# Performance work log

Hardware: AMD Instinct MI355X
Metric: run time of the kernel (lower is better)

## Reference

```python
import jax, jax.numpy as jnp
import numpy as np
import math

N_HEAD = 12


def setup_inputs() -> dict:
    key = jax.random.key(0)
    k1, k2, k3 = jax.random.split(key, 3)
    B, T, C = 4, 2048, 768
    x = jax.random.normal(k1, (B, T, C), dtype=jnp.float32)
    W = jax.random.normal(k2, (C, 3 * C), dtype=jnp.float32) * 0.02
    b = jax.random.normal(k3, (3 * C,), dtype=jnp.float32) * 0.02
    return {"x": x, "W": W, "b": b}


def reference(x, W, b):
    B, T, C = x.shape
    H = N_HEAD
    d = C // H
    qkv = x @ W + b                                # [B,T,3C]
    q, k, v = jnp.split(qkv, 3, axis=-1)           # each [B,T,C]
    q = q.reshape(B, T, H, d).transpose(0, 2, 1, 3)  # [B,H,T,d]
    k = k.reshape(B, T, H, d).transpose(0, 2, 1, 3)
    v = v.reshape(B, T, H, d).transpose(0, 2, 1, 3)
    # NOTE: source multiplies by sqrt(d) (not divides) -- faithful reproduction.
    att = jnp.einsum('bhqd,bhkd->bhqk', q, k) * (1.0 * math.sqrt(d))
    causal = jnp.tril(jnp.ones((T, T), dtype=bool))  # [T,T]
    att = jnp.where(causal[None, None, :, :], att, -jnp.inf)
    att = jax.nn.softmax(att, axis=-1)
    y = jnp.einsum('bhqk,bhkd->bhqd', att, v)      # [B,H,T,d]
    y = y.transpose(0, 2, 1, 3).reshape(B, T, C)   # [B,T,C]
    return y
```

## Files before the change

kernel.cpp:

```cpp
#include <hip/hip_runtime.h>
#include <math.h>

#define B_ 4
#define T_ 2048
#define C_ 768
#define H_ 12
#define D_ 64
#define N3C (3*C_)
#define BH_ (B_*H_)
#define QSCALE 11.5415603f

typedef float f32x4 __attribute__((ext_vector_type(4)));
typedef _Float16 f16x8 __attribute__((ext_vector_type(8)));
typedef _Float16 f16x4v __attribute__((ext_vector_type(4)));
typedef unsigned short ushort_t;

__device__ __forceinline__ void async16(const void* g, void* l) {
    __builtin_amdgcn_global_load_lds(
        (const __attribute__((address_space(1))) unsigned int*)(g),
        (__attribute__((address_space(3))) unsigned int*)(l),
        16, 0, 0);
}

__device__ __forceinline__ unsigned pk_f16(float a, float b) {
    __fp16 r2[2];
    *(__fp16 __attribute__((ext_vector_type(2)))*)r2 = __builtin_amdgcn_cvt_pkrtz(a, b);
    return *(unsigned*)r2;
}

__global__ __launch_bounds__(256) void conv_xw(const float* __restrict__ x,
                                               const float* __restrict__ W,
                                               _Float16* __restrict__ Xh,
                                               _Float16* __restrict__ Wh)
{
    __shared__ float tile[64][65];
    int bid = blockIdx.x;
    int tid = threadIdx.x;
    if (bid < 3072) {
        int idx = bid * 256 + tid;
        const float4 a = *reinterpret_cast<const float4*>(&x[(size_t)idx * 8]);
        const float4 b = *reinterpret_cast<const float4*>(&x[(size_t)idx * 8 + 4]);
        f16x8 o = {(_Float16)a.x, (_Float16)a.y, (_Float16)a.z, (_Float16)a.w,
                   (_Float16)b.x, (_Float16)b.y, (_Float16)b.z, (_Float16)b.w};
        *reinterpret_cast<f16x8*>(&Xh[(size_t)idx * 8]) = o;
    } else {
        int b2 = bid - 3072;
        int n0 = (b2 % 36) * 64, k0 = (b2 / 36) * 64;
        #pragma unroll
        for (int t = 0; t < 16; ++t) {
            int c = t * 256 + tid;
            int kr = c >> 6, nc = c & 63;
            tile[kr][nc] = W[(size_t)(k0 + kr) * N3C + n0 + nc];
        }
        __syncthreads();
        #pragma unroll
        for (int t = 0; t < 16; ++t) {
            int c = t * 256 + tid;
            int nr = c >> 6, kc = c & 63;
            Wh[(size_t)(n0 + nr) * C_ + k0 + kc] = (_Float16)tile[kc][nr];
        }
    }
}

__global__ __launch_bounds__(256) void qkv_gemm(const _Float16* __restrict__ Xh,
                                                const _Float16* __restrict__ Wh,
                                                const float* __restrict__ bias,
                                                _Float16* __restrict__ Qf,
                                                _Float16* __restrict__ Kf,
                                                _Float16* __restrict__ Vt)
{
    __shared__ __align__(16) ushort_t SMEM[2 * 2 * 128 * 64];

    int tid = threadIdx.x, lane = tid & 63, w = tid >> 6;
    int wm = w >> 1, wn = w & 1;
    int l15 = lane & 15, l4 = lane >> 4;
    int srow = lane >> 3;
    int scol = (((lane & 7) ^ srow)) << 3;

    int wg = blockIdx.x;
    int l = (wg & 7) * 144 + (wg >> 3);
    int mt = l / 18, nt = l % 18;
    int row0 = mt * 128, col0 = nt * 128;

    f32x4 acc[4][4];
    #pragma unroll
    for (int i = 0; i < 4; ++i)
        #pragma unroll
        for (int j = 0; j < 4; ++j)
            acc[i][j] = f32x4{0.f, 0.f, 0.f, 0.f};

    #pragma unroll
    for (int j = 0; j < 4; ++j) {
        int rowb = w * 32 + j * 8;
        async16(Xh + (size_t)(row0 + rowb + srow) * C_ + scol, &SMEM[rowb * 64]);
        async16(Wh + (size_t)(col0 + rowb + srow) * C_ + scol, &SMEM[8192 + rowb * 64]);
    }
    __syncthreads();

    int cur = 0;
    for (int it = 0; it < 12; ++it) {
        int nxt = cur ^ 1;
        int k0n = (it + 1) * 64;
        bool pf = (it + 1 < 12);
        const char* AsC = (const char*)(SMEM + cur * 16384);
        const char* BsC = AsC + 16384;
        ushort_t* An = SMEM + nxt * 16384;
        ushort_t* Bn = An + 8192;

        if (pf) {
            #pragma unroll
            for (int j = 0; j < 2; ++j) {
                int rowb = w * 32 + j * 8;
                async16(Xh + (size_t)(row0 + rowb + srow) * C_ + k0n + scol, &An[rowb * 64]);
                async16(Wh + (size_t)(col0 + rowb + srow) * C_ + k0n + scol, &Bn[rowb * 64]);
            }
        }
        f16x8 bfr[4][2];
        #pragma unroll
        for (int n = 0; n < 4; ++n) {
            int r = wn * 64 + n * 16 + l15;
            #pragma unroll
            for (int kk = 0; kk < 2; ++kk)
                bfr[n][kk] = *reinterpret_cast<const f16x8*>(BsC + r * 128 + ((kk * 64 + l4 * 16) ^ ((r & 7) << 4)));
        }
        {
            f16x8 af[2][2];
            #pragma unroll
            for (int m = 0; m < 2; ++m) {
                int r = wm * 64 + m * 16 + l15;
                #pragma unroll
                for (int kk = 0; kk < 2; ++kk)
                    af[m][kk] = *reinterpret_cast<const f16x8*>(AsC + r * 128 + ((kk * 64 + l4 * 16) ^ ((r & 7) << 4)));
            }
            #pragma unroll
            for (int kk = 0; kk < 2; ++kk)
                #pragma unroll
                for (int m = 0; m < 2; ++m)
                    #pragma unroll
                    for (int n = 0; n < 4; ++n)
                        acc[m][n] = __builtin_amdgcn_mfma_f32_16x16x32_f16(af[m][kk], bfr[n][kk], acc[m][n], 0, 0, 0);
        }

        if (pf) {
            #pragma unroll
            for (int j = 2; j < 4; ++j) {
                int rowb = w * 32 + j * 8;
                async16(Xh + (size_t)(row0 + rowb + srow) * C_ + k0n + scol, &An[rowb * 64]);
                async16(Wh + (size_t)(col0 + rowb + srow) * C_ + k0n + scol, &Bn[rowb * 64]);
            }
        }
        {
            f16x8 af[2][2];
            #pragma unroll
            for (int m = 0; m < 2; ++m) {
                int r = wm * 64 + (m + 2) * 16 + l15;
                #pragma unroll
                for (int kk = 0; kk < 2; ++kk)
                    af[m][kk] = *reinterpret_cast<const f16x8*>(AsC + r * 128 + ((kk * 64 + l4 * 16) ^ ((r & 7) << 4)));
            }
            #pragma unroll
            for (int kk = 0; kk < 2; ++kk)
                #pragma unroll
                for (int m = 0; m < 2; ++m)
                    #pragma unroll
                    for (int n = 0; n < 4; ++n)
                        acc[m + 2][n] = __builtin_amdgcn_mfma_f32_16x16x32_f16(af[m][kk], bfr[n][kk], acc[m + 2][n], 0, 0, 0);
        }

        __syncthreads();
        cur = nxt;
    }

    char* EB = (char*)SMEM;
    int p = col0 / C_;

    if (p < 2) {
        #pragma unroll
        for (int n = 0; n < 4; ++n) {
            int col = wn * 64 + n * 16 + l15;
            float bv = bias[col0 + col];
            #pragma unroll
            for (int m = 0; m < 4; ++m) {
                #pragma unroll
                for (int r = 0; r < 4; ++r) {
                    int row = wm * 64 + m * 16 + l4 * 4 + r;
                    float v = acc[m][n][r] + bv;
                    if (p == 0) v *= QSCALE;
                    int off = row * 256 + ((col * 2) ^ ((row & 7) << 4));
                    *reinterpret_cast<_Float16*>(EB + off) = (_Float16)v;
                }
            }
        }
        __syncthreads();
        int ti = tid >> 1, half = tid & 1;
        int grow = row0 + ti;
        int bq = grow >> 11, t = grow & (T_ - 1);
        int rem = (col0 + half * 64) - p * C_;
        int hh = rem >> 6;
        _Float16* dst = (p == 0 ? Qf : Kf) + ((size_t)(bq * H_ + hh) * T_ + t) * D_;
        #pragma unroll
        for (int u = 0; u < 8; ++u) {
            int off = ti * 256 + ((half * 128 + u * 16) ^ ((ti & 7) << 4));
            *reinterpret_cast<uint4*>((char*)dst + u * 16) = *reinterpret_cast<const uint4*>(EB + off);
        }
    } else {
        #pragma unroll
        for (int n = 0; n < 4; ++n) {
            int col = wn * 64 + n * 16 + l15;
            float bv = bias[col0 + col];
            #pragma unroll
            for (int m = 0; m < 4; ++m) {
                int row = wm * 64 + m * 16 + l4 * 4;
                uint2 pk;
                pk.x = pk_f16(acc[m][n][0] + bv, acc[m][n][1] + bv);
                pk.y = pk_f16(acc[m][n][2] + bv, acc[m][n][3] + bv);
                int off = col * 256 + ((row * 2) ^ ((col & 15) << 4));
                *reinterpret_cast<uint2*>(EB + off) = pk;
            }
        }
        __syncthreads();
        int dcol = tid >> 1, half = tid & 1;
        int rem = (col0 + dcol) - 1536;
        int hh = rem >> 6, dd = rem & 63;
        int bq = row0 >> 11, t0 = row0 & (T_ - 1);
        _Float16* dst = Vt + ((size_t)(bq * H_ + hh) * D_ + dd) * T_ + t0 + half * 64;
        #pragma unroll
        for (int u = 0; u < 8; ++u) {
            int off = dcol * 256 + ((half * 128 + u * 16) ^ ((dcol & 15) << 4));
            *reinterpret_cast<uint4*>((char*)dst + u * 16) = *reinterpret_cast<const uint4*>(EB + off);
        }
    }
}

__device__ const unsigned char ITEM_QT[24] = {15,15,7,14,14,13,13,6,12,12,11,11,5,10,10,9,9,4,8,8,3,2,1,0};
__device__ const unsigned char ITEM_CH[24] = { 0, 1,0, 0, 1, 0, 1,0, 0, 1, 0, 1,0, 0, 1,0,1,0,0,1,0,0,0,0};

__global__ __launch_bounds__(256, 4) void attn(const _Float16* __restrict__ Qf,
                                               const _Float16* __restrict__ Kf,
                                               const _Float16* __restrict__ Vt,
                                               float* __restrict__ out,
                                               ushort_t* __restrict__ Oph,
                                               float* __restrict__ ML)
{
    __shared__ __align__(16) char smem[32768];
    ushort_t* lds = (ushort_t*)smem;

    int tid = threadIdx.x, lane = tid & 63, w = tid >> 6;
    int l15 = lane & 15, l4 = lane >> 4;
    int bid = blockIdx.x;
    int rank = bid / BH_;
    int bh = bid % BH_;
    int qt = ITEM_QT[rank];
    int ch = ITEM_CH[rank];
    int b = bh / H_, h = bh % H_;
    int q0 = qt * 128;

    int it0 = (qt < 8 || ch == 0) ? 0 : (qt + 1);
    int it1 = (qt >= 8 && ch == 0) ? (qt + 1) : (2 * qt + 2);

    f16x8 qf[2][2];
    #pragma unroll
    for (int qs = 0; qs < 2; ++qs) {
        int q = q0 + w * 32 + qs * 16 + l15;
        const _Float16* ph = Qf + ((size_t)bh * T_ + q) * D_;
        qf[qs][0] = *reinterpret_cast<const f16x8*>(ph + l4 * 8);
        qf[qs][1] = *reinterpret_cast<const f16x8*>(ph + 32 + l4 * 8);
    }

    f32x4 yacc[2][4];
    #pragma unroll
    for (int qs = 0; qs < 2; ++qs)
        #pragma unroll
        for (int dt = 0; dt < 4; ++dt)
            yacc[qs][dt] = f32x4{0.f, 0.f, 0.f, 0.f};
    float m_run[2] = {-INFINITY, -INFINITY};
    float l_run[2] = {0.f, 0.f};

    int srow = lane >> 3;
    int scol = ((lane & 7) ^ srow) << 3;

    const _Float16* kp[2];
    const _Float16* vp[2];
    #pragma unroll
    for (int j = 0; j < 2; ++j) {
        int ldsrow = (w * 2 + j) * 8 + srow;
        int kperm = ((ldsrow >> 4) & 1) * 32 + ((ldsrow >> 2) & 3) * 8 + ((ldsrow >> 5) << 2) + (ldsrow & 3);
        kp[j] = Kf + ((size_t)bh * T_ + it0 * 64 + kperm) * D_ + scol;
        vp[j] = Vt + ((size_t)bh * D_ + ldsrow) * T_ + it0 * 64 + scol;
    }

    #pragma unroll
    for (int j = 0; j < 2; ++j) {
        ushort_t* dK = lds + (w * 2 + j) * 512;
        async16(kp[j], dK);
        async16(vp[j], dK + 4096);
        kp[j] += 64 * D_;
        vp[j] += 64;
    }
    __syncthreads();

    int cur = 0;
    for (int it = it0; it < it1; ++it) {
        int k0 = it * 64;
        int nxt = cur ^ 1;
        if (it + 1 < it1) {
            #pragma unroll
            for (int j = 0; j < 2; ++j) {
                ushort_t* dK = lds + nxt * 8192 + (w * 2 + j) * 512;
                async16(kp[j], dK);
                async16(vp[j], dK + 4096);
                kp[j] += 64 * D_;
                vp[j] += 64;
            }
        }

        if (k0 <= q0 + w * 32 + 31) {
            const char* KHc = (const char*)(lds + cur * 8192);
            const char* VSc = KHc + 8192;
            f16x8 pa[2][2];
            f32x4 sa[2][4];
            #pragma unroll
            for (int qs = 0; qs < 2; ++qs)
                #pragma unroll
                for (int i = 0; i < 4; ++i) sa[qs][i] = f32x4{0.f, 0.f, 0.f, 0.f};

            __builtin_amdgcn_s_setprio(1);
            #pragma unroll
            for (int kt = 0; kt < 4; ++kt) {
                int krow = kt * 16 + l15;
                int swz = (krow & 7) << 4;
                #pragma unroll
                for (int dh = 0; dh < 2; ++dh) {
                    f16x8 kf = *reinterpret_cast<const f16x8*>(KHc + krow * 128 + ((dh * 64 + l4 * 16) ^ swz));
                    sa[0][kt] = __builtin_amdgcn_mfma_f32_16x16x32_f16(kf, qf[0][dh], sa[0][kt], 0, 0, 0);
                    sa[1][kt] = __builtin_amdgcn_mfma_f32_16x16x32_f16(kf, qf[1][dh], sa[1][kt], 0, 0, 0);
                }
            }
            __builtin_amdgcn_s_setprio(0);

            int kml = k0 + l4 * 8;
            #pragma unroll
            for (int qs = 0; qs < 2; ++qs) {
                if (it >= 2 * qt) {
                    int qg = q0 + w * 32 + qs * 16 + l15;
                    #pragma unroll
                    for (int kt = 0; kt < 4; ++kt)
                        #pragma unroll
                        for (int r = 0; r < 4; ++r) {
                            int kact = kml + ((kt & 1) << 5) + ((kt >> 1) << 2) + r;
                            if (kact > qg) sa[qs][kt][r] = -INFINITY;
                        }
                }

                float mx = sa[qs][0][0];
                #pragma unroll
                for (int kt = 0; kt < 4; ++kt)
                    #pragma unroll
                    for (int r = 0; r < 4; ++r) mx = fmaxf(mx, sa[qs][kt][r]);
                mx = fmaxf(mx, __shfl_xor(mx, 16));
                mx = fmaxf(mx, __shfl_xor(mx, 32));

                float mn;
                if (__all(mx <= m_run[qs] + 8.0f)) {
                    mn = m_run[qs];
                } else {
                    mn = fmaxf(m_run[qs], mx);
                    float sc = exp2f(m_run[qs] - mn);
                    m_run[qs] = mn;
                    l_run[qs] *= sc;
                    #pragma unroll
                    for (int dt = 0; dt < 4; ++dt) yacc[qs][dt] *= sc;
                }

                float p[4][4];
                float rs = 0.f;
                #pragma unroll
                for (int kt = 0; kt < 4; ++kt)
                    #pragma unroll
                    for (int r = 0; r < 4; ++r) {
                        p[kt][r] = exp2f(sa[qs][kt][r] - mn);
                        rs += p[kt][r];
                    }
                l_run[qs] += rs;

                union { uint4 u; f16x8 hh8; } c0, c1;
                c0.u.x = pk_f16(p[0][0], p[0][1]);
                c0.u.y = pk_f16(p[0][2], p[0][3]);
                c0.u.z = pk_f16(p[2][0], p[2][1]);
                c0.u.w = pk_f16(p[2][2], p[2][3]);
                c1.u.x = pk_f16(p[1][0], p[1][1]);
                c1.u.y = pk_f16(p[1][2], p[1][3]);
                c1.u.z = pk_f16(p[3][0], p[3][1]);
                c1.u.w = pk_f16(p[3][2], p[3][3]);
                pa[qs][0] = c0.hh8;
                pa[qs][1] = c1.hh8;
            }

            __builtin_amdgcn_s_setprio(1);
            #pragma unroll
            for (int dt = 0; dt < 4; ++dt) {
                int vrow = dt * 16 + l15;
                int vswz = (vrow & 7) << 4;
                #pragma unroll
                for (int kk = 0; kk < 2; ++kk) {
                    f16x8 vf = *reinterpret_cast<const f16x8*>(VSc + vrow * 128 + ((kk * 64 + l4 * 16) ^ vswz));
                    yacc[0][dt] = __builtin_amdgcn_mfma_f32_16x16x32_f16(vf, pa[0][kk], yacc[0][dt], 0, 0, 0);
                    yacc[1][dt] = __builtin_amdgcn_mfma_f32_16x16x32_f16(vf, pa[1][kk], yacc[1][dt], 0, 0, 0);
                }
            }
            __builtin_amdgcn_s_setprio(0);
        }
        __syncthreads();
        cur = nxt;
    }

    #pragma unroll
    for (int qs = 0; qs < 2; ++qs) {
        l_run[qs] += __shfl_xor(l_run[qs], 16);
        l_run[qs] += __shfl_xor(l_run[qs], 32);
    }

    bool split = (qt >= 8);
    if (split && l4 == 0) {
        float* mlp = ML + (((size_t)bh * 8 + (qt - 8)) * 2 + ch) * 256;
        #pragma unroll
        for (int qs = 0; qs < 2; ++qs) {
            int ql = w * 32 + qs * 16 + l15;
            mlp[ql] = m_run[qs];
            mlp[128 + ql] = l_run[qs];
        }
    }

    char* otB = smem;
    #pragma unroll
    for (int qs = 0; qs < 2; ++qs) {
        float inv = 1.0f / l_run[qs];
        int rq = w * 32 + qs * 16 + l15;
        int swz = (rq & 15) << 4;
        #pragma unroll
        for (int dt = 0; dt < 4; ++dt) {
            float4 v4;
            v4.x = yacc[qs][dt][0] * inv;
            v4.y = yacc[qs][dt][1] * inv;
            v4.z = yacc[qs][dt][2] * inv;
            v4.w = yacc[qs][dt][3] * inv;
            *reinterpret_cast<float4*>(otB + rq * 256 + ((dt * 64 + l4 * 16) ^ swz)) = v4;
        }
    }
    __syncthreads();
    {
        int rr = tid >> 1, cb = (tid & 1) * 128;
        int swz = (rr & 15) << 4;
        if (!split) {
            size_t ob = ((size_t)(b * T_ + q0 + rr)) * C_ + h * D_ + (tid & 1) * 32;
            #pragma unroll
            for (int u = 0; u < 8; ++u) {
                float4 v = *reinterpret_cast<const float4*>(otB + rr * 256 + ((cb + u * 16) ^ swz));
                *reinterpret_cast<float4*>(&out[ob + u * 4]) = v;
            }
        } else {
            ushort_t* dst = Oph + (((size_t)bh * 8 + (qt - 8)) * 2 + ch) * 8192 + rr * 64 + (tid & 1) * 32;
            #pragma unroll
            for (int u = 0; u < 8; ++u) {
                float4 v = *reinterpret_cast<const float4*>(otB + rr * 256 + ((cb + u * 16) ^ swz));
                uint2 pk;
                pk.x = pk_f16(v.x, v.y);
                pk.y = pk_f16(v.z, v.w);
                *reinterpret_cast<uint2*>(&dst[u * 4]) = pk;
            }
        }
    }
}

__global__ __launch_bounds__(256) void merge(const ushort_t* __restrict__ Oph,
                                             const float* __restrict__ ML,
                                             float* __restrict__ out)
{
    int gid = blockIdx.x * 256 + threadIdx.x;
    int row = gid >> 4, seg = gid & 15;
    int q = row & 127, qt8 = (row >> 7) & 7, bh = row >> 10;

    size_t mbase = ((size_t)bh * 8 + qt8) * 2 * 256;
    float m1 = ML[mbase + q],       l1 = ML[mbase + 128 + q];
    float m2 = ML[mbase + 256 + q], l2 = ML[mbase + 256 + 128 + q];
    float m = fmaxf(m1, m2);
    float w1 = exp2f(m1 - m) * l1, w2 = exp2f(m2 - m) * l2;
    float inv = 1.0f / (w1 + w2);
    w1 *= inv; w2 *= inv;

    size_t obase = ((size_t)bh * 8 + qt8) * 2 * 8192 + q * 64 + seg * 4;
    f16x4v o1 = *reinterpret_cast<const f16x4v*>(&Oph[obase]);
    f16x4v o2 = *reinterpret_cast<const f16x4v*>(&Oph[obase + 8192]);
    float4 r;
    r.x = (float)o1[0] * w1 + (float)o2[0] * w2;
    r.y = (float)o1[1] * w1 + (float)o2[1] * w2;
    r.z = (float)o1[2] * w1 + (float)o2[2] * w2;
    r.w = (float)o1[3] * w1 + (float)o2[3] * w2;

    int b = bh / H_, h = bh % H_;
    int t = (qt8 + 8) * 128 + q;
    *reinterpret_cast<float4*>(&out[((size_t)(b * T_ + t)) * C_ + h * D_ + seg * 4]) = r;
}

extern "C" void kernel_launch(void* const* d_in, const int* in_sizes, int n_in,
                              void* d_out, int out_size, void* d_ws, size_t ws_size,
                              hipStream_t stream)
{
    const float* x    = (const float*)d_in[0];
    const float* W    = (const float*)d_in[1];
    const float* bias = (const float*)d_in[2];

    const size_t per = (size_t)BH_ * T_ * D_;
    _Float16* Qf = (_Float16*)d_ws;
    _Float16* Kf = Qf + per;
    _Float16* Vt = Kf + per;
    _Float16* Xh = Vt + per;
    _Float16* Wh = Xh + (size_t)8192 * C_;
    ushort_t* Oph = (ushort_t*)(Wh + (size_t)N3C * C_);
    float*    ML  = (float*)(Oph + (size_t)48 * 8 * 2 * 8192);

    conv_xw<<<dim3(3072 + 432), 256, 0, stream>>>(x, W, Xh, Wh);
    qkv_gemm<<<dim3(64 * 18), 256, 0, stream>>>(Xh, Wh, bias, Qf, Kf, Vt);
    attn<<<dim3(24 * BH_), 256, 0, stream>>>(Qf, Kf, Vt, (float*)d_out, Oph, ML);
    merge<<<dim3(49152 * 16 / 256), 256, 0, stream>>>(Oph, ML, (float*)d_out);
}
```

Measured before the change: 127.1 us.

## Split long causal query tiles into up to four KV chunks for better balance

Query tiles at index 4 and up now have their KV range split into 1 to 4 chunks that grow with tile length, replacing the old 2-way split used only for tiles 8 and up. The attention grid grows from 24 to 40 items per batch-head, and a lookup table orders the items longest first. The merge kernel now combines a variable number of partials using their max and sum statistics. The aim is to even out per-block work and remove the tail caused by long causal rows, at the cost of more fp16 partial traffic and a larger merge pass.

```diff
diff --git a/kernel.cpp b/kernel.cpp
--- a/kernel.cpp
+++ b/kernel.cpp
@@ -232,8 +232,16 @@
     }
 }
 
-__device__ const unsigned char ITEM_QT[24] = {15,15,7,14,14,13,13,6,12,12,11,11,5,10,10,9,9,4,8,8,3,2,1,0};
-__device__ const unsigned char ITEM_CH[24] = { 0, 1,0, 0, 1, 0, 1,0, 0, 1, 0, 1,0, 0, 1,0,1,0,0,1,0,0,0,0};
+__device__ const unsigned char ITEM_QT[40] = {
+    15,15,15,15,14,14,11,11,11,10, 7, 7, 3,
+    14,14,13,13,13,13,12,12,10,10, 9, 9, 6, 6,
+    12,12, 9, 8, 8, 8, 5, 5, 2,
+     4, 4, 1, 0};
+__device__ const unsigned char ITEM_CH[40] = {
+     0, 1, 2, 3, 1, 3, 0, 1, 2, 2, 0, 1, 0,
+     0, 2, 0, 1, 2, 3, 1, 3, 0, 1, 1, 2, 0, 1,
+     0, 2, 0, 0, 1, 2, 0, 1, 0,
+     0, 1, 0, 0};
 
 __global__ __launch_bounds__(256, 4) void attn(const _Float16* __restrict__ Qf,
                                                const _Float16* __restrict__ Kf,
@@ -255,8 +263,10 @@
     int b = bh / H_, h = bh % H_;
     int q0 = qt * 128;
 
-    int it0 = (qt < 8 || ch == 0) ? 0 : (qt + 1);
-    int it1 = (qt >= 8 && ch == 0) ? (qt + 1) : (2 * qt + 2);
+    int ntl = 2 * qt + 2;
+    int nc  = (qt >= 4) ? ((2 * qt + 9) >> 3) : 1;
+    int it0 = ch * ntl / nc;
+    int it1 = (ch + 1) * ntl / nc;
 
     f16x8 qf[2][2];
     #pragma unroll
@@ -420,9 +430,10 @@
         l_run[qs] += __shfl_xor(l_run[qs], 32);
     }
 
-    bool split = (qt >= 8);
+    bool split = (qt >= 4);
+    size_t item = split ? (((size_t)bh * 12 + (qt - 4)) * 4 + ch) : 0;
     if (split && l4 == 0) {
-        float* mlp = ML + (((size_t)bh * 8 + (qt - 8)) * 2 + ch) * 256;
+        float* mlp = ML + item * 256;
         #pragma unroll
         for (int qs = 0; qs < 2; ++qs) {
             int ql = w * 32 + qs * 16 + l15;
@@ -434,7 +445,7 @@
     char* otB = smem;
     #pragma unroll
     for (int qs = 0; qs < 2; ++qs) {
-        float inv = 1.0f / l_run[qs];
+        float inv = (l_run[qs] > 0.f) ? (1.0f / l_run[qs]) : 0.f;
         int rq = w * 32 + qs * 16 + l15;
         int swz = (rq & 15) << 4;
         #pragma unroll
@@ -459,7 +470,7 @@
                 *reinterpret_cast<float4*>(&out[ob + u * 4]) = v;
             }
         } else {
-            ushort_t* dst = Oph + (((size_t)bh * 8 + (qt - 8)) * 2 + ch) * 8192 + rr * 64 + (tid & 1) * 32;
+            ushort_t* dst = Oph + item * 8192 + rr * 64 + (tid & 1) * 32;
             #pragma unroll
             for (int u = 0; u < 8; ++u) {
                 float4 v = *reinterpret_cast<const float4*>(otB + rr * 256 + ((cb + u * 16) ^ swz));
@@ -478,27 +489,44 @@
 {
     int gid = blockIdx.x * 256 + threadIdx.x;
     int row = gid >> 4, seg = gid & 15;
-    int q = row & 127, qt8 = (row >> 7) & 7, bh = row >> 10;
-
-    size_t mbase = ((size_t)bh * 8 + qt8) * 2 * 256;
-    float m1 = ML[mbase + q],       l1 = ML[mbase + 128 + q];
-    float m2 = ML[mbase + 256 + q], l2 = ML[mbase + 256 + 128 + q];
-    float m = fmaxf(m1, m2);
-    float w1 = exp2f(m1 - m) * l1, w2 = exp2f(m2 - m) * l2;
-    float inv = 1.0f / (w1 + w2);
-    w1 *= inv; w2 *= inv;
-
-    size_t obase = ((size_t)bh * 8 + qt8) * 2 * 8192 + q * 64 + seg * 4;
-    f16x4v o1 = *reinterpret_cast<const f16x4v*>(&Oph[obase]);
-    f16x4v o2 = *reinterpret_cast<const f16x4v*>(&Oph[obase + 8192]);
-    float4 r;
-    r.x = (float)o1[0] * w1 + (float)o2[0] * w2;
-    r.y = (float)o1[1] * w1 + (float)o2[1] * w2;
-    r.z = (float)o1[2] * w1 + (float)o2[2] * w2;
-    r.w = (float)o1[3] * w1 + (float)o2[3] * w2;
+    int q = row & 127, qtm = (row >> 7) % 12, bh = row / 1536;
+    int qt = qtm + 4;
+    int nc = (2 * qt + 9) >> 3;
+
+    size_t ibase = ((size_t)bh * 12 + qtm) * 4;
+    float mm[4], ll[4];
+    float ms = -INFINITY;
+    #pragma unroll
+    for (int c = 0; c < 4; ++c) {
+        if (c < nc) {
+            mm[c] = ML[(ibase + c) * 256 + q];
+            ll[c] = ML[(ibase + c) * 256 + 128 + q];
+            ms = fmaxf(ms, mm[c]);
+        }
+    }
+    float wsum = 0.f, wt[4];
+    #pragma unroll
+    for (int c = 0; c < 4; ++c) {
+        wt[c] = (c < nc) ? exp2f(mm[c] - ms) * ll[c] : 0.f;
+        wsum += wt[c];
+    }
+    float inv = 1.0f / wsum;
+
+    float4 r = {0.f, 0.f, 0.f, 0.f};
+    #pragma unroll
+    for (int c = 0; c < 4; ++c) {
+        if (c < nc) {
+            float wc = wt[c] * inv;
+            f16x4v o = *reinterpret_cast<const f16x4v*>(&Oph[(ibase + c) * 8192 + q * 64 + seg * 4]);
+            r.x += (float)o[0] * wc;
+            r.y += (float)o[1] * wc;
+            r.z += (float)o[2] * wc;
+            r.w += (float)o[3] * wc;
+        }
+    }
 
     int b = bh / H_, h = bh % H_;
-    int t = (qt8 + 8) * 128 + q;
+    int t = qt * 128 + q;
     *reinterpret_cast<float4*>(&out[((size_t)(b * T_ + t)) * C_ + h * D_ + seg * 4]) = r;
 }
 
@@ -517,10 +545,10 @@
     _Float16* Xh = Vt + per;
     _Float16* Wh = Xh + (size_t)8192 * C_;
     ushort_t* Oph = (ushort_t*)(Wh + (size_t)N3C * C_);
-    float*    ML  = (float*)(Oph + (size_t)48 * 8 * 2 * 8192);
+    float*    ML  = (float*)(Oph + (size_t)48 * 12 * 4 * 8192);
 
     conv_xw<<<dim3(3072 + 432), 256, 0, stream>>>(x, W, Xh, Wh);
     qkv_gemm<<<dim3(64 * 18), 256, 0, stream>>>(Xh, Wh, bias, Qf, Kf, Vt);
-    attn<<<dim3(24 * BH_), 256, 0, stream>>>(Qf, Kf, Vt, (float*)d_out, Oph, ML);
-    merge<<<dim3(49152 * 16 / 256), 256, 0, stream>>>(Oph, ML, (float*)d_out);
-}
+    attn<<<dim3(40 * BH_), 256, 0, stream>>>(Qf, Kf, Vt, (float*)d_out, Oph, ML);
+    merge<<<dim3(48 * 12 * 128 * 16 / 256), 256, 0, stream>>>(Oph, ML, (float*)d_out);
+}
```

Result: slower. 134.3 us (+5.6%).
